# Performance work log

Measured on AMD Instinct MI355X. Metric: run time of the kernel, lower is better.

## Reference

```python
import jax, jax.numpy as jnp
import numpy as np

HEADS = 8
LN_EPS = 1e-5


def _elu_plus_one(t):
    # F.elu(x) + 1 == exp(x) for x<0, x+1 for x>=0
    return jax.nn.elu(t) + 1.0


def setup_inputs() -> dict:
    key = jax.random.key(0)
    k1, k2, k3 = jax.random.split(key, 3)
    dim = 256
    x = jax.random.normal(k1, (16, dim, 64, 64), dtype=jnp.float32)
    w_qkv = jax.random.normal(k2, (3 * dim, dim), dtype=jnp.float32) * 0.02
    w_out = jax.random.normal(k3, (dim, dim), dtype=jnp.float32) * 0.02
    ln_gamma = jnp.ones((dim,), dtype=jnp.float32)
    ln_beta = jnp.zeros((dim,), dtype=jnp.float32)
    return {"x": x, "w_qkv": w_qkv, "w_out": w_out, "ln_gamma": ln_gamma, "ln_beta": ln_beta}


def reference(x, w_qkv, w_out, ln_gamma, ln_beta):
    b, c, h, w = x.shape
    hd = c // HEADS
    n = h * w
    # 1x1 conv == per-pixel matmul over channels
    qkv = jnp.einsum('bchw,oc->bohw', x, w_qkv)  # [b, 3c, h, w]
    q, k, v = jnp.split(qkv, 3, axis=1)
    q = q.reshape(b, HEADS, hd, n)
    k = k.reshape(b, HEADS, hd, n)
    v = v.reshape(b, HEADS, hd, n)
    qk = _elu_plus_one(q)
    kk = _elu_plus_one(k)
    # channel-wise kv reduction over spatial positions (NOT an outer product)
    kv = jnp.sum(kk * v, axis=-1, keepdims=True)        # [b, heads, hd, 1]
    denom = jnp.maximum(jnp.sum(kk, axis=-1, keepdims=True), 1e-6)
    out = qk * (kv / denom)                              # [b, heads, hd, n]
    out = out.reshape(b, c, h, w)
    out = jnp.einsum('bchw,oc->bohw', out, w_out)        # 1x1 output conv
    # LayerNorm over channel dim (module permutes to NHWC first)
    t = jnp.transpose(out, (0, 2, 3, 1))                 # [b, h, w, c]
    mu = jnp.mean(t, axis=-1, keepdims=True)
    var = jnp.mean(jnp.square(t - mu), axis=-1, keepdims=True)
    t = (t - mu) * jax.lax.rsqrt(var + LN_EPS) * ln_gamma + ln_beta
    return jnp.transpose(t, (0, 3, 1, 2))
```

## Files before the change

kernel.cpp:

```cpp
#include <hip/hip_runtime.h>


#define NB 16
#define NC 256
#define NN 4096
#define LN_EPS 1e-5f
#define IOSCALE (1.0f/1024.0f)

typedef _Float16 f16;
typedef _Float16 f16x8 __attribute__((ext_vector_type(8)));
typedef _Float16 f16x4v __attribute__((ext_vector_type(4)));
typedef float f32x4 __attribute__((ext_vector_type(4)));

typedef __attribute__((address_space(1))) const unsigned int* as1cu32;
typedef __attribute__((address_space(3))) unsigned int* as3u32;

__device__ __forceinline__ void gload16(const void* g, void* l) {
  __builtin_amdgcn_global_load_lds((as1cu32)g, (as3u32)l, 16, 0, 0);
}

__device__ __forceinline__ float elu1(float x) {
  return x > 0.f ? x + 1.f : __expf(x);
}

__global__ __launch_bounds__(256) void k_convw(const float* __restrict__ w,
                                               f16* __restrict__ wh, int n) {
  int i = blockIdx.x * 256 + threadIdx.x;
  if (i < n) wh[i] = (f16)w[i];
}

__global__ __launch_bounds__(256) void k_transpose(const float* __restrict__ x,
                                                   f16* __restrict__ xh) {
  __shared__ float t[64 * 65];
  const int b = blockIdx.z, c0 = blockIdx.y * 64, n0 = blockIdx.x * 64;
  const int tid = threadIdx.x;
#pragma unroll
  for (int i = 0; i < 4; ++i) {
    int lin = tid + i * 256;
    int r = lin >> 4;
    int cg = lin & 15;
    const float4 v = *reinterpret_cast<const float4*>(
        &x[((size_t)(b * NC + c0 + r)) * NN + n0 + cg * 4]);
    t[r * 65 + cg * 4 + 0] = v.x;
    t[r * 65 + cg * 4 + 1] = v.y;
    t[r * 65 + cg * 4 + 2] = v.z;
    t[r * 65 + cg * 4 + 3] = v.w;
  }
  __syncthreads();
#pragma unroll
  for (int i = 0; i < 4; ++i) {
    int lin = tid + i * 256;
    int nr = lin >> 4;
    int cg = lin & 15;
    f16x4v h;
    h[0] = (f16)t[(cg * 4 + 0) * 65 + nr];
    h[1] = (f16)t[(cg * 4 + 1) * 65 + nr];
    h[2] = (f16)t[(cg * 4 + 2) * 65 + nr];
    h[3] = (f16)t[(cg * 4 + 3) * 65 + nr];
    *reinterpret_cast<f16x4v*>(&xh[((size_t)(b * NN + n0 + nr)) * NC + c0 + cg * 4]) = h;
  }
}

__global__ __launch_bounds__(256) void k_gemm_q(const f16* __restrict__ xh,
                                                const f16* __restrict__ wh,
                                                f16* __restrict__ qh) {
  __shared__ __align__(16) f16 At[128 * 64];
  __shared__ __align__(16) f16 Bt[128 * 64];
  const int b = blockIdx.z;
  const int n0 = blockIdx.x * 128;
  const int o0 = blockIdx.y * 128;
  const int tid = threadIdx.x;
  const int lane = tid & 63;
  const int wv = tid >> 6;
  const int wn = wv >> 1, wo = wv & 1;
  const int l15 = lane & 15, lg = lane >> 4;
  const int srow = lane >> 3;
  const int sch = (lane & 7) * 8;

  f32x4 acc[4][4] = {};

  for (int ks = 0; ks < 4; ++ks) {
    const int c0 = ks * 64;
#pragma unroll
    for (int it = 0; it < 4; ++it) {
      const int seg = wv * 4 + it;
      const int row = seg * 8 + srow;
      gload16(xh + ((size_t)(b * NN + n0 + row)) * NC + c0 + sch, At + seg * 512);
      gload16(wh + (size_t)(o0 + row) * NC + c0 + sch, Bt + seg * 512);
    }
    __syncthreads();
#pragma unroll
    for (int kk = 0; kk < 2; ++kk) {
      const int kb = kk * 32 + lg * 8;
      f16x8 af[4], bf[4];
#pragma unroll
      for (int m = 0; m < 4; ++m)
        af[m] = *(const f16x8*)(At + (wn * 64 + m * 16 + l15) * 64 + kb);
#pragma unroll
      for (int n = 0; n < 4; ++n)
        bf[n] = *(const f16x8*)(Bt + (wo * 64 + n * 16 + l15) * 64 + kb);
#pragma unroll
      for (int m = 0; m < 4; ++m)
#pragma unroll
        for (int n = 0; n < 4; ++n)
          acc[m][n] = __builtin_amdgcn_mfma_f32_16x16x32_f16(af[m], bf[n], acc[m][n], 0, 0, 0);
    }
    __syncthreads();
  }
#pragma unroll
  for (int m = 0; m < 4; ++m) {
    const int nr = n0 + wn * 64 + m * 16 + lg * 4;
#pragma unroll
    for (int n = 0; n < 4; ++n) {
      const int oc = o0 + wo * 64 + n * 16 + l15;
#pragma unroll
      for (int j = 0; j < 4; ++j)
        qh[((size_t)(b * NN + nr + j)) * NC + oc] = (f16)elu1(acc[m][n][j]);
    }
  }
}

__global__ __launch_bounds__(256) void k_gemm_kv(const f16* __restrict__ xh,
                                                 const f16* __restrict__ wh,
                                                 float* __restrict__ kv,
                                                 float* __restrict__ den) {
  __shared__ __align__(16) f16 At[128 * 64];
  __shared__ __align__(16) f16 Bt[128 * 64];
  const int b = blockIdx.z;
  const int n0 = blockIdx.x * 128;
  const int cc0 = blockIdx.y * 64;
  const int tid = threadIdx.x;
  const int lane = tid & 63;
  const int wv = tid >> 6;
  const int l15 = lane & 15, lg = lane >> 4;
  const int srow = lane >> 3;
  const int sch = (lane & 7) * 8;

  f32x4 acc[2][8] = {};

  for (int ks = 0; ks < 4; ++ks) {
    const int c0 = ks * 64;
#pragma unroll
    for (int it = 0; it < 4; ++it) {
      const int seg = wv * 4 + it;
      const int row = seg * 8 + srow;
      gload16(xh + ((size_t)(b * NN + n0 + row)) * NC + c0 + sch, At + seg * 512);
      const int wrow = row < 64 ? 256 + cc0 + row : 512 + cc0 + (row - 64);
      gload16(wh + (size_t)wrow * NC + c0 + sch, Bt + seg * 512);
    }
    __syncthreads();
#pragma unroll
    for (int kk = 0; kk < 2; ++kk) {
      const int kb = kk * 32 + lg * 8;
      f16x8 af[2], bf[8];
#pragma unroll
      for (int m = 0; m < 2; ++m)
        af[m] = *(const f16x8*)(At + (wv * 32 + m * 16 + l15) * 64 + kb);
#pragma unroll
      for (int f = 0; f < 8; ++f)
        bf[f] = *(const f16x8*)(Bt + (f * 16 + l15) * 64 + kb);
#pragma unroll
      for (int m = 0; m < 2; ++m)
#pragma unroll
        for (int f = 0; f < 8; ++f)
          acc[m][f] = __builtin_amdgcn_mfma_f32_16x16x32_f16(af[m], bf[f], acc[m][f], 0, 0, 0);
    }
    __syncthreads();
  }
  float pkv[4], pden[4];
#pragma unroll
  for (int f = 0; f < 4; ++f) { pkv[f] = 0.f; pden[f] = 0.f; }
#pragma unroll
  for (int f = 0; f < 4; ++f)
#pragma unroll
    for (int m = 0; m < 2; ++m)
#pragma unroll
      for (int j = 0; j < 4; ++j) {
        const float kkv = elu1(acc[m][f][j]);
        pkv[f] += kkv * acc[m][f + 4][j];
        pden[f] += kkv;
      }
#pragma unroll
  for (int f = 0; f < 4; ++f) {
    pkv[f] += __shfl_xor(pkv[f], 16, 64);
    pkv[f] += __shfl_xor(pkv[f], 32, 64);
    pden[f] += __shfl_xor(pden[f], 16, 64);
    pden[f] += __shfl_xor(pden[f], 32, 64);
  }
  if (lane < 16) {
#pragma unroll
    for (int f = 0; f < 4; ++f) {
      const int c = cc0 + f * 16 + lane;
      atomicAdd(&kv[b * NC + c], pkv[f]);
      atomicAdd(&den[b * NC + c], pden[f]);
    }
  }
}

__global__ __launch_bounds__(256) void k_ws(const float* __restrict__ wout,
                                            const float* __restrict__ kv,
                                            const float* __restrict__ den,
                                            f16* __restrict__ wsc) {
  int i = blockIdx.x * 256 + threadIdx.x;
  int c = i & 255;
  int o = (i >> 8) & 255;
  int b = i >> 16;
  float s = kv[b * 256 + c] / fmaxf(den[b * 256 + c], 1e-6f);
  wsc[i] = (f16)(wout[o * 256 + c] * s * 1024.0f);
}

__global__ __launch_bounds__(256) void k_gemm2_ln(const f16* __restrict__ wsc,
                                                  const f16* __restrict__ qh,
                                                  const float* __restrict__ gamma,
                                                  const float* __restrict__ beta,
                                                  float* __restrict__ out) {
  __shared__ __align__(16) f16 At[256 * 64];
  __shared__ __align__(16) f16 Bt[64 * 64];
  __shared__ float red1[4][64];
  __shared__ float red2[4][64];
  __shared__ float smu[64], srs[64];
  const int b = blockIdx.y;
  const int n0 = blockIdx.x * 64;
  const int tid = threadIdx.x;
  const int lane = tid & 63;
  const int wv = tid >> 6;
  const int l15 = lane & 15, lg = lane >> 4;
  const int srow = lane >> 3;
  const int sch = (lane & 7) * 8;
  const f16* wsb = wsc + (size_t)b * NC * NC;

  f32x4 acc[4][4] = {};

  for (int ks = 0; ks < 4; ++ks) {
    const int c0 = ks * 64;
#pragma unroll
    for (int it = 0; it < 8; ++it) {
      const int seg = wv * 8 + it;
      const int row = seg * 8 + srow;
      gload16(wsb + (size_t)row * NC + c0 + sch, At + seg * 512);
    }
#pragma unroll
    for (int it = 0; it < 2; ++it) {
      const int seg = wv * 2 + it;
      const int row = seg * 8 + srow;
      gload16(qh + ((size_t)(b * NN + n0 + row)) * NC + c0 + sch, Bt + seg * 512);
    }
    __syncthreads();
#pragma unroll
    for (int kk = 0; kk < 2; ++kk) {
      const int kb = kk * 32 + lg * 8;
      f16x8 af[4], bf[4];
#pragma unroll
      for (int m = 0; m < 4; ++m)
        af[m] = *(const f16x8*)(At + (wv * 64 + m * 16 + l15) * 64 + kb);
#pragma unroll
      for (int f = 0; f < 4; ++f)
        bf[f] = *(const f16x8*)(Bt + (f * 16 + l15) * 64 + kb);
#pragma unroll
      for (int m = 0; m < 4; ++m)
#pragma unroll
        for (int f = 0; f < 4; ++f)
          acc[m][f] = __builtin_amdgcn_mfma_f32_16x16x32_f16(af[m], bf[f], acc[m][f], 0, 0, 0);
    }
    __syncthreads();
  }
  float s1[4] = {0, 0, 0, 0}, s2[4] = {0, 0, 0, 0};
#pragma unroll
  for (int f = 0; f < 4; ++f)
#pragma unroll
    for (int m = 0; m < 4; ++m)
#pragma unroll
      for (int j = 0; j < 4; ++j) {
        const float v = acc[m][f][j];
        s1[f] += v;
        s2[f] += v * v;
      }
#pragma unroll
  for (int f = 0; f < 4; ++f) {
    s1[f] += __shfl_xor(s1[f], 16, 64);
    s1[f] += __shfl_xor(s1[f], 32, 64);
    s2[f] += __shfl_xor(s2[f], 16, 64);
    s2[f] += __shfl_xor(s2[f], 32, 64);
  }
  if (lane < 16) {
#pragma unroll
    for (int f = 0; f < 4; ++f) {
      red1[wv][f * 16 + lane] = s1[f];
      red2[wv][f * 16 + lane] = s2[f];
    }
  }
  __syncthreads();
  if (tid < 64) {
    const float a1 = red1[0][tid] + red1[1][tid] + red1[2][tid] + red1[3][tid];
    const float a2 = red2[0][tid] + red2[1][tid] + red2[2][tid] + red2[3][tid];
    const float mu = a1 * (IOSCALE / 256.f);
    const float e2 = a2 * (IOSCALE * IOSCALE / 256.f);
    smu[tid] = mu;
    srs[tid] = rsqrtf(e2 - mu * mu + LN_EPS);
  }
  __syncthreads();
#pragma unroll
  for (int m = 0; m < 4; ++m) {
    const int ob = wv * 64 + m * 16 + lg * 4;
#pragma unroll
    for (int j = 0; j < 4; ++j) {
      const int o = ob + j;
      const float g = gamma[o], be = beta[o];
#pragma unroll
      for (int f = 0; f < 4; ++f) {
        const int col = f * 16 + l15;
        const float v = acc[m][f][j] * IOSCALE;
        out[((size_t)(b * NC + o)) * NN + n0 + col] = (v - smu[col]) * srs[col] * g + be;
      }
    }
  }
}

extern "C" void kernel_launch(void* const* d_in, const int* in_sizes, int n_in,
                              void* d_out, int out_size, void* d_ws, size_t ws_size,
                              hipStream_t stream) {
  const float* x = (const float*)d_in[0];
  const float* w_qkv = (const float*)d_in[1];
  const float* w_out = (const float*)d_in[2];
  const float* ln_g = (const float*)d_in[3];
  const float* ln_b = (const float*)d_in[4];
  float* out = (float*)d_out;

  char* wsb = (char*)d_ws;
  const size_t OFF_WH = 0;
  const size_t OFF_XH = OFF_WH + 393216;
  const size_t OFF_QH = OFF_XH + 33554432;
  const size_t OFF_KV = OFF_QH + 33554432;
  const size_t OFF_DEN = OFF_KV + 16384;
  const size_t OFF_WSC = OFF_DEN + 16384;

  f16* wh = (f16*)(wsb + OFF_WH);
  f16* xh = (f16*)(wsb + OFF_XH);
  f16* qh = (f16*)(wsb + OFF_QH);
  float* kv = (float*)(wsb + OFF_KV);
  float* den = (float*)(wsb + OFF_DEN);
  f16* wsc = (f16*)(wsb + OFF_WSC);

  hipMemsetAsync(kv, 0, 2 * 16384, stream);

  k_convw<<<768, 256, 0, stream>>>(w_qkv, wh, 768 * 256);
  k_transpose<<<dim3(64, 4, 16), 256, 0, stream>>>(x, xh);
  k_gemm_q<<<dim3(32, 2, 16), 256, 0, stream>>>(xh, wh, qh);
  k_gemm_kv<<<dim3(32, 4, 16), 256, 0, stream>>>(xh, wh, kv, den);
  k_ws<<<4096, 256, 0, stream>>>(w_out, kv, den, wsc);
  k_gemm2_ln<<<dim3(64, 16), 256, 0, stream>>>(wsc, qh, ln_g, ln_b, out);
}
```

Before: 103.2 us.

## Fuse transpose, Q and KV GEMMs into one kernel reading fp32 input

```diff
diff --git a/kernel.cpp b/kernel.cpp
--- a/kernel.cpp
+++ b/kernel.cpp
@@ -9,7 +9,6 @@
 
 typedef _Float16 f16;
 typedef _Float16 f16x8 __attribute__((ext_vector_type(8)));
-typedef _Float16 f16x4v __attribute__((ext_vector_type(4)));
 typedef float f32x4 __attribute__((ext_vector_type(4)));
 
 typedef __attribute__((address_space(1))) const unsigned int* as1cu32;
@@ -23,162 +22,93 @@
   return x > 0.f ? x + 1.f : __expf(x);
 }
 
-__global__ __launch_bounds__(256) void k_convw(const float* __restrict__ w,
-                                               f16* __restrict__ wh, int n) {
+__global__ __launch_bounds__(256) void k_init(const float* __restrict__ w,
+                                              f16* __restrict__ wh,
+                                              float* __restrict__ kvden) {
   int i = blockIdx.x * 256 + threadIdx.x;
-  if (i < n) wh[i] = (f16)w[i];
-}
-
-__global__ __launch_bounds__(256) void k_transpose(const float* __restrict__ x,
-                                                   f16* __restrict__ xh) {
-  __shared__ float t[64 * 65];
-  const int b = blockIdx.z, c0 = blockIdx.y * 64, n0 = blockIdx.x * 64;
-  const int tid = threadIdx.x;
-#pragma unroll
-  for (int i = 0; i < 4; ++i) {
-    int lin = tid + i * 256;
-    int r = lin >> 4;
-    int cg = lin & 15;
-    const float4 v = *reinterpret_cast<const float4*>(
-        &x[((size_t)(b * NC + c0 + r)) * NN + n0 + cg * 4]);
-    t[r * 65 + cg * 4 + 0] = v.x;
-    t[r * 65 + cg * 4 + 1] = v.y;
-    t[r * 65 + cg * 4 + 2] = v.z;
-    t[r * 65 + cg * 4 + 3] = v.w;
-  }
-  __syncthreads();
-#pragma unroll
-  for (int i = 0; i < 4; ++i) {
-    int lin = tid + i * 256;
-    int nr = lin >> 4;
-    int cg = lin & 15;
-    f16x4v h;
-    h[0] = (f16)t[(cg * 4 + 0) * 65 + nr];
-    h[1] = (f16)t[(cg * 4 + 1) * 65 + nr];
-    h[2] = (f16)t[(cg * 4 + 2) * 65 + nr];
-    h[3] = (f16)t[(cg * 4 + 3) * 65 + nr];
-    *reinterpret_cast<f16x4v*>(&xh[((size_t)(b * NN + n0 + nr)) * NC + c0 + cg * 4]) = h;
-  }
-}
-
-__global__ __launch_bounds__(256) void k_gemm_q(const f16* __restrict__ xh,
+  if (i < 768 * 256) wh[i] = (f16)w[i];
+  if (i < 8192) kvden[i] = 0.f;
+}
+
+__global__ __launch_bounds__(512, 2) void k_qkv(const float* __restrict__ x,
                                                 const f16* __restrict__ wh,
-                                                f16* __restrict__ qh) {
-  __shared__ __align__(16) f16 At[128 * 64];
-  __shared__ __align__(16) f16 Bt[128 * 64];
-  const int b = blockIdx.z;
-  const int n0 = blockIdx.x * 128;
-  const int o0 = blockIdx.y * 128;
-  const int tid = threadIdx.x;
-  const int lane = tid & 63;
-  const int wv = tid >> 6;
-  const int wn = wv >> 1, wo = wv & 1;
-  const int l15 = lane & 15, lg = lane >> 4;
-  const int srow = lane >> 3;
-  const int sch = (lane & 7) * 8;
-
-  f32x4 acc[4][4] = {};
-
-  for (int ks = 0; ks < 4; ++ks) {
-    const int c0 = ks * 64;
-#pragma unroll
-    for (int it = 0; it < 4; ++it) {
-      const int seg = wv * 4 + it;
-      const int row = seg * 8 + srow;
-      gload16(xh + ((size_t)(b * NN + n0 + row)) * NC + c0 + sch, At + seg * 512);
-      gload16(wh + (size_t)(o0 + row) * NC + c0 + sch, Bt + seg * 512);
-    }
-    __syncthreads();
-#pragma unroll
-    for (int kk = 0; kk < 2; ++kk) {
-      const int kb = kk * 32 + lg * 8;
-      f16x8 af[4], bf[4];
-#pragma unroll
-      for (int m = 0; m < 4; ++m)
-        af[m] = *(const f16x8*)(At + (wn * 64 + m * 16 + l15) * 64 + kb);
-#pragma unroll
-      for (int n = 0; n < 4; ++n)
-        bf[n] = *(const f16x8*)(Bt + (wo * 64 + n * 16 + l15) * 64 + kb);
-#pragma unroll
-      for (int m = 0; m < 4; ++m)
-#pragma unroll
-        for (int n = 0; n < 4; ++n)
-          acc[m][n] = __builtin_amdgcn_mfma_f32_16x16x32_f16(af[m], bf[n], acc[m][n], 0, 0, 0);
-    }
-    __syncthreads();
-  }
-#pragma unroll
-  for (int m = 0; m < 4; ++m) {
-    const int nr = n0 + wn * 64 + m * 16 + lg * 4;
-#pragma unroll
-    for (int n = 0; n < 4; ++n) {
-      const int oc = o0 + wo * 64 + n * 16 + l15;
-#pragma unroll
-      for (int j = 0; j < 4; ++j)
-        qh[((size_t)(b * NN + nr + j)) * NC + oc] = (f16)elu1(acc[m][n][j]);
-    }
-  }
-}
-
-__global__ __launch_bounds__(256) void k_gemm_kv(const f16* __restrict__ xh,
-                                                 const f16* __restrict__ wh,
-                                                 float* __restrict__ kv,
-                                                 float* __restrict__ den) {
-  __shared__ __align__(16) f16 At[128 * 64];
-  __shared__ __align__(16) f16 Bt[128 * 64];
-  const int b = blockIdx.z;
-  const int n0 = blockIdx.x * 128;
-  const int cc0 = blockIdx.y * 64;
+                                                f16* __restrict__ qh,
+                                                float* __restrict__ kv,
+                                                float* __restrict__ den) {
+  __shared__ __align__(16) f16 A[64 * 264];
+  const int b = blockIdx.y;
+  const int n0 = blockIdx.x * 64;
   const int tid = threadIdx.x;
   const int lane = tid & 63;
   const int wv = tid >> 6;
   const int l15 = lane & 15, lg = lane >> 4;
-  const int srow = lane >> 3;
-  const int sch = (lane & 7) * 8;
-
-  f32x4 acc[2][8] = {};
-
-  for (int ks = 0; ks < 4; ++ks) {
-    const int c0 = ks * 64;
-#pragma unroll
-    for (int it = 0; it < 4; ++it) {
-      const int seg = wv * 4 + it;
-      const int row = seg * 8 + srow;
-      gload16(xh + ((size_t)(b * NN + n0 + row)) * NC + c0 + sch, At + seg * 512);
-      const int wrow = row < 64 ? 256 + cc0 + row : 512 + cc0 + (row - 64);
-      gload16(wh + (size_t)wrow * NC + c0 + sch, Bt + seg * 512);
-    }
-    __syncthreads();
-#pragma unroll
-    for (int kk = 0; kk < 2; ++kk) {
-      const int kb = kk * 32 + lg * 8;
-      f16x8 af[2], bf[8];
-#pragma unroll
-      for (int m = 0; m < 2; ++m)
-        af[m] = *(const f16x8*)(At + (wv * 32 + m * 16 + l15) * 64 + kb);
-#pragma unroll
-      for (int f = 0; f < 8; ++f)
-        bf[f] = *(const f16x8*)(Bt + (f * 16 + l15) * 64 + kb);
-#pragma unroll
-      for (int m = 0; m < 2; ++m)
-#pragma unroll
-        for (int f = 0; f < 8; ++f)
-          acc[m][f] = __builtin_amdgcn_mfma_f32_16x16x32_f16(af[m], bf[f], acc[m][f], 0, 0, 0);
-    }
-    __syncthreads();
-  }
-  float pkv[4], pden[4];
-#pragma unroll
-  for (int f = 0; f < 4; ++f) { pkv[f] = 0.f; pden[f] = 0.f; }
+
+  {
+    const int c = tid >> 1;
+    const int nh = (tid & 1) * 32;
+    const float* xp = x + ((size_t)(b * NC + c)) * NN + n0 + nh;
+#pragma unroll
+    for (int i = 0; i < 8; ++i) {
+      const float4 v4 = *reinterpret_cast<const float4*>(xp + i * 4);
+      const int nb = nh + i * 4;
+      A[(nb + 0) * 264 + c] = (f16)v4.x;
+      A[(nb + 1) * 264 + c] = (f16)v4.y;
+      A[(nb + 2) * 264 + c] = (f16)v4.z;
+      A[(nb + 3) * 264 + c] = (f16)v4.w;
+    }
+  }
+  __syncthreads();
+
+  const int ng = wv >> 2;
+  const int cb = (wv & 3) * 64;
+
+  f32x4 aq[2][4] = {}, ak[2][4] = {}, av[2][4] = {};
+  const f16* arow0 = A + (ng * 32 + l15) * 264;
+  const f16* arow1 = arow0 + 16 * 264;
+  const f16* wl = wh + (size_t)(cb + l15) * NC + lg * 8;
+
+#pragma unroll 2
+  for (int kq = 0; kq < 8; ++kq) {
+    const int kb = kq * 32 + lg * 8;
+    const f16x8 a0 = *(const f16x8*)(arow0 + kb);
+    const f16x8 a1 = *(const f16x8*)(arow1 + kb);
+#pragma unroll
+    for (int f = 0; f < 4; ++f) {
+      const f16* wf = wl + f * 16 * NC + kq * 32;
+      const f16x8 bq = *(const f16x8*)(wf);
+      const f16x8 bk = *(const f16x8*)(wf + 256 * NC);
+      const f16x8 bv = *(const f16x8*)(wf + 512 * NC);
+      aq[0][f] = __builtin_amdgcn_mfma_f32_16x16x32_f16(a0, bq, aq[0][f], 0, 0, 0);
+      aq[1][f] = __builtin_amdgcn_mfma_f32_16x16x32_f16(a1, bq, aq[1][f], 0, 0, 0);
+      ak[0][f] = __builtin_amdgcn_mfma_f32_16x16x32_f16(a0, bk, ak[0][f], 0, 0, 0);
+      ak[1][f] = __builtin_amdgcn_mfma_f32_16x16x32_f16(a1, bk, ak[1][f], 0, 0, 0);
+      av[0][f] = __builtin_amdgcn_mfma_f32_16x16x32_f16(a0, bv, av[0][f], 0, 0, 0);
+      av[1][f] = __builtin_amdgcn_mfma_f32_16x16x32_f16(a1, bv, av[1][f], 0, 0, 0);
+    }
+  }
+
+#pragma unroll
+  for (int m = 0; m < 2; ++m) {
+    const int nr = n0 + ng * 32 + m * 16 + lg * 4;
+#pragma unroll
+    for (int f = 0; f < 4; ++f) {
+      const int oc = cb + f * 16 + l15;
+#pragma unroll
+      for (int j = 0; j < 4; ++j)
+        qh[((size_t)(b * NN + nr + j)) * NC + oc] = (f16)elu1(aq[m][f][j]);
+    }
+  }
+
+  float pkv[4] = {0.f, 0.f, 0.f, 0.f}, pden[4] = {0.f, 0.f, 0.f, 0.f};
 #pragma unroll
   for (int f = 0; f < 4; ++f)
 #pragma unroll
     for (int m = 0; m < 2; ++m)
 #pragma unroll
       for (int j = 0; j < 4; ++j) {
-        const float kkv = elu1(acc[m][f][j]);
-        pkv[f] += kkv * acc[m][f + 4][j];
-        pden[f] += kkv;
+        const float kk = elu1(ak[m][f][j]);
+        pkv[f] += kk * av[m][f][j];
+        pden[f] += kk;
       }
 #pragma unroll
   for (int f = 0; f < 4; ++f) {
@@ -190,9 +120,8 @@
   if (lane < 16) {
 #pragma unroll
     for (int f = 0; f < 4; ++f) {
-      const int c = cc0 + f * 16 + lane;
-      atomicAdd(&kv[b * NC + c], pkv[f]);
-      atomicAdd(&den[b * NC + c], pden[f]);
+      atomicAdd(&kv[b * NC + cb + f * 16 + lane], pkv[f]);
+      atomicAdd(&den[b * NC + cb + f * 16 + lane], pden[f]);
     }
   }
 }
@@ -328,25 +257,19 @@
 
   char* wsb = (char*)d_ws;
   const size_t OFF_WH = 0;
-  const size_t OFF_XH = OFF_WH + 393216;
-  const size_t OFF_QH = OFF_XH + 33554432;
+  const size_t OFF_QH = OFF_WH + 393216;
   const size_t OFF_KV = OFF_QH + 33554432;
   const size_t OFF_DEN = OFF_KV + 16384;
   const size_t OFF_WSC = OFF_DEN + 16384;
 
   f16* wh = (f16*)(wsb + OFF_WH);
-  f16* xh = (f16*)(wsb + OFF_XH);
   f16* qh = (f16*)(wsb + OFF_QH);
   float* kv = (float*)(wsb + OFF_KV);
   float* den = (float*)(wsb + OFF_DEN);
   f16* wsc = (f16*)(wsb + OFF_WSC);
 
-  hipMemsetAsync(kv, 0, 2 * 16384, stream);
-
-  k_convw<<<768, 256, 0, stream>>>(w_qkv, wh, 768 * 256);
-  k_transpose<<<dim3(64, 4, 16), 256, 0, stream>>>(x, xh);
-  k_gemm_q<<<dim3(32, 2, 16), 256, 0, stream>>>(xh, wh, qh);
-  k_gemm_kv<<<dim3(32, 4, 16), 256, 0, stream>>>(xh, wh, kv, den);
+  k_init<<<768, 256, 0, stream>>>(w_qkv, wh, kv);
+  k_qkv<<<dim3(64, 16), 512, 0, stream>>>(x, wh, qh, kv, den);
   k_ws<<<4096, 256, 0, stream>>>(w_out, kv, den, wsc);
   k_gemm2_ln<<<dim3(64, 16), 256, 0, stream>>>(wsc, qh, ln_g, ln_b, out);
 }
```

After: 148.5 us. +43.9%, slower.

## XOR-swizzle LDS tiles in GEMM kernels and fold kv/den memset into init

Applied to the files above, without the earlier changes.

```diff
diff --git a/kernel.cpp b/kernel.cpp
--- a/kernel.cpp
+++ b/kernel.cpp
@@ -23,10 +23,16 @@
   return x > 0.f ? x + 1.f : __expf(x);
 }
 
-__global__ __launch_bounds__(256) void k_convw(const float* __restrict__ w,
-                                               f16* __restrict__ wh, int n) {
+__device__ __forceinline__ int swz(int row, int unit) {
+  return row * 64 + (((unit) ^ (row & 7)) << 3);
+}
+
+__global__ __launch_bounds__(256) void k_init(const float* __restrict__ w,
+                                              f16* __restrict__ wh,
+                                              float* __restrict__ kvden) {
   int i = blockIdx.x * 256 + threadIdx.x;
-  if (i < n) wh[i] = (f16)w[i];
+  if (i < 768 * 256) wh[i] = (f16)w[i];
+  if (i < 8192) kvden[i] = 0.f;
 }
 
 __global__ __launch_bounds__(256) void k_transpose(const float* __restrict__ x,
@@ -75,7 +81,7 @@
   const int wn = wv >> 1, wo = wv & 1;
   const int l15 = lane & 15, lg = lane >> 4;
   const int srow = lane >> 3;
-  const int sch = (lane & 7) * 8;
+  const int ssrc = ((lane & 7) ^ srow) * 8;
 
   f32x4 acc[4][4] = {};
 
@@ -85,20 +91,20 @@
     for (int it = 0; it < 4; ++it) {
       const int seg = wv * 4 + it;
       const int row = seg * 8 + srow;
-      gload16(xh + ((size_t)(b * NN + n0 + row)) * NC + c0 + sch, At + seg * 512);
-      gload16(wh + (size_t)(o0 + row) * NC + c0 + sch, Bt + seg * 512);
+      gload16(xh + ((size_t)(b * NN + n0 + row)) * NC + c0 + ssrc, At + seg * 512);
+      gload16(wh + (size_t)(o0 + row) * NC + c0 + ssrc, Bt + seg * 512);
     }
     __syncthreads();
 #pragma unroll
     for (int kk = 0; kk < 2; ++kk) {
-      const int kb = kk * 32 + lg * 8;
+      const int ku = kk * 4 + lg;
       f16x8 af[4], bf[4];
 #pragma unroll
       for (int m = 0; m < 4; ++m)
-        af[m] = *(const f16x8*)(At + (wn * 64 + m * 16 + l15) * 64 + kb);
+        af[m] = *(const f16x8*)(At + swz(wn * 64 + m * 16 + l15, ku));
 #pragma unroll
       for (int n = 0; n < 4; ++n)
-        bf[n] = *(const f16x8*)(Bt + (wo * 64 + n * 16 + l15) * 64 + kb);
+        bf[n] = *(const f16x8*)(Bt + swz(wo * 64 + n * 16 + l15, ku));
 #pragma unroll
       for (int m = 0; m < 4; ++m)
 #pragma unroll
@@ -134,7 +140,7 @@
   const int wv = tid >> 6;
   const int l15 = lane & 15, lg = lane >> 4;
   const int srow = lane >> 3;
-  const int sch = (lane & 7) * 8;
+  const int ssrc = ((lane & 7) ^ srow) * 8;
 
   f32x4 acc[2][8] = {};
 
@@ -144,21 +150,21 @@
     for (int it = 0; it < 4; ++it) {
       const int seg = wv * 4 + it;
       const int row = seg * 8 + srow;
-      gload16(xh + ((size_t)(b * NN + n0 + row)) * NC + c0 + sch, At + seg * 512);
+      gload16(xh + ((size_t)(b * NN + n0 + row)) * NC + c0 + ssrc, At + seg * 512);
       const int wrow = row < 64 ? 256 + cc0 + row : 512 + cc0 + (row - 64);
-      gload16(wh + (size_t)wrow * NC + c0 + sch, Bt + seg * 512);
+      gload16(wh + (size_t)wrow * NC + c0 + ssrc, Bt + seg * 512);
     }
     __syncthreads();
 #pragma unroll
     for (int kk = 0; kk < 2; ++kk) {
-      const int kb = kk * 32 + lg * 8;
+      const int ku = kk * 4 + lg;
       f16x8 af[2], bf[8];
 #pragma unroll
       for (int m = 0; m < 2; ++m)
-        af[m] = *(const f16x8*)(At + (wv * 32 + m * 16 + l15) * 64 + kb);
+        af[m] = *(const f16x8*)(At + swz(wv * 32 + m * 16 + l15, ku));
 #pragma unroll
       for (int f = 0; f < 8; ++f)
-        bf[f] = *(const f16x8*)(Bt + (f * 16 + l15) * 64 + kb);
+        bf[f] = *(const f16x8*)(Bt + swz(f * 16 + l15, ku));
 #pragma unroll
       for (int m = 0; m < 2; ++m)
 #pragma unroll
@@ -167,18 +173,16 @@
     }
     __syncthreads();
   }
-  float pkv[4], pden[4];
-#pragma unroll
-  for (int f = 0; f < 4; ++f) { pkv[f] = 0.f; pden[f] = 0.f; }
+  float pkv[4] = {0.f, 0.f, 0.f, 0.f}, pden[4] = {0.f, 0.f, 0.f, 0.f};
 #pragma unroll
   for (int f = 0; f < 4; ++f)
 #pragma unroll
     for (int m = 0; m < 2; ++m)
 #pragma unroll
       for (int j = 0; j < 4; ++j) {
-        const float kkv = elu1(acc[m][f][j]);
-        pkv[f] += kkv * acc[m][f + 4][j];
-        pden[f] += kkv;
+        const float kk = elu1(acc[m][f][j]);
+        pkv[f] += kk * acc[m][f + 4][j];
+        pden[f] += kk;
       }
 #pragma unroll
   for (int f = 0; f < 4; ++f) {
@@ -226,7 +230,7 @@
   const int wv = tid >> 6;
   const int l15 = lane & 15, lg = lane >> 4;
   const int srow = lane >> 3;
-  const int sch = (lane & 7) * 8;
+  const int ssrc = ((lane & 7) ^ srow) * 8;
   const f16* wsb = wsc + (size_t)b * NC * NC;
 
   f32x4 acc[4][4] = {};
@@ -237,25 +241,25 @@
     for (int it = 0; it < 8; ++it) {
       const int seg = wv * 8 + it;
       const int row = seg * 8 + srow;
-      gload16(wsb + (size_t)row * NC + c0 + sch, At + seg * 512);
+      gload16(wsb + (size_t)row * NC + c0 + ssrc, At + seg * 512);
     }
 #pragma unroll
     for (int it = 0; it < 2; ++it) {
       const int seg = wv * 2 + it;
       const int row = seg * 8 + srow;
-      gload16(qh + ((size_t)(b * NN + n0 + row)) * NC + c0 + sch, Bt + seg * 512);
+      gload16(qh + ((size_t)(b * NN + n0 + row)) * NC + c0 + ssrc, Bt + seg * 512);
     }
     __syncthreads();
 #pragma unroll
     for (int kk = 0; kk < 2; ++kk) {
-      const int kb = kk * 32 + lg * 8;
+      const int ku = kk * 4 + lg;
       f16x8 af[4], bf[4];
 #pragma unroll
       for (int m = 0; m < 4; ++m)
-        af[m] = *(const f16x8*)(At + (wv * 64 + m * 16 + l15) * 64 + kb);
+        af[m] = *(const f16x8*)(At + swz(wv * 64 + m * 16 + l15, ku));
 #pragma unroll
       for (int f = 0; f < 4; ++f)
-        bf[f] = *(const f16x8*)(Bt + (f * 16 + l15) * 64 + kb);
+        bf[f] = *(const f16x8*)(Bt + swz(f * 16 + l15, ku));
 #pragma unroll
       for (int m = 0; m < 4; ++m)
 #pragma unroll
@@ -341,9 +345,7 @@
   float* den = (float*)(wsb + OFF_DEN);
   f16* wsc = (f16*)(wsb + OFF_WSC);
 
-  hipMemsetAsync(kv, 0, 2 * 16384, stream);
-
-  k_convw<<<768, 256, 0, stream>>>(w_qkv, wh, 768 * 256);
+  k_init<<<768, 256, 0, stream>>>(w_qkv, wh, kv);
   k_transpose<<<dim3(64, 4, 16), 256, 0, stream>>>(x, xh);
   k_gemm_q<<<dim3(32, 2, 16), 256, 0, stream>>>(xh, wh, qh);
   k_gemm_kv<<<dim3(32, 4, 16), 256, 0, stream>>>(xh, wh, kv, den);
```

New measurement: 95.79 us. -7.2%, faster.
